# Performance work log

Hardware: AMD Instinct MI355X
Metric: run time of the kernel (lower is better)

The kernel has to match this reference:

```python
import jax, jax.numpy as jnp
import numpy as np

NUM_HEADS = 12
HEAD_DIM = 64


def setup_inputs() -> dict:
    key = jax.random.key(0)
    ks = jax.random.split(key, 8)
    B, S, D, M = 8, 1024, 768, 8
    scale = 0.02
    return {
        "hidden_states": jax.random.normal(ks[0], (B, S, D), jnp.float32),
        "memory": jax.random.normal(ks[1], (1, M, D), jnp.float32) * scale,
        "Wq": jax.random.normal(ks[2], (D, D), jnp.float32) * scale,
        "bq": jnp.zeros((D,), jnp.float32),
        "Wk": jax.random.normal(ks[3], (D, D), jnp.float32) * scale,
        "bk": jnp.zeros((D,), jnp.float32),
        "Wv": jax.random.normal(ks[4], (D, D), jnp.float32) * scale,
        "bv": jnp.zeros((D,), jnp.float32),
    }


def _split_heads(x):
    # (B, S, D) -> (B, H, S, Dh)
    B, S, _ = x.shape
    return x.reshape(B, S, NUM_HEADS, HEAD_DIM).transpose(0, 2, 1, 3)


def reference(hidden_states, memory, Wq, bq, Wk, bk, Wv, bv):
    B, S, D = hidden_states.shape
    # prepend? no: memory tokens are concatenated AFTER hidden_states on token dim
    mem = jnp.broadcast_to(memory, (B,) + memory.shape[1:])
    with_memory = jnp.concatenate([hidden_states, mem], axis=1)  # (B, S+M, D)

    # torch nn.Linear: x @ W.T + b
    q = _split_heads(hidden_states @ Wq.T + bq)   # (B, H, S,   Dh)
    k = _split_heads(with_memory @ Wk.T + bk)     # (B, H, S+M, Dh)
    v = _split_heads(with_memory @ Wv.T + bv)     # (B, H, S+M, Dh)

    scaling = 1.0 / np.sqrt(HEAD_DIM).astype(np.float32)
    scores = jnp.einsum("bhqd,bhkd->bhqk", q, k) * scaling
    probs = jax.nn.softmax(scores, axis=-1)  # dropout is identity in eval
    ctx = jnp.einsum("bhqk,bhkd->bhqd", probs, v)  # (B, H, S, Dh)
    ctx = ctx.transpose(0, 2, 1, 3).reshape(B, S, D)
    return ctx
```

## Files before the change

kernel.cpp:

```cpp
#include <hip/hip_runtime.h>

typedef unsigned short ushort_t;
typedef __attribute__((ext_vector_type(8))) short bf16x8;
typedef __attribute__((ext_vector_type(4))) short s16x4;
typedef __attribute__((ext_vector_type(4))) float f32x4;

#define BATCH 8
#define SEQ   1024
#define MEMT  8
#define LREAL 1032
#define LPAD  1152
#define DMODEL 768
#define NH    12
#define DH    64

#define CEXP 0.18033688011112042f

__device__ __forceinline__ ushort_t f2b(float x) {
  union { float f; unsigned u; } c; c.f = x;
  unsigned u = c.u;
  unsigned r = (u + 0x7fffu + ((u >> 16) & 1u)) >> 16;
  return (ushort_t)r;
}

#if defined(__has_builtin)
#if __has_builtin(__builtin_amdgcn_global_load_lds)
#define HAVE_GLL 1
#endif
#if __has_builtin(__builtin_amdgcn_exp2f)
#define EXP2F(x) __builtin_amdgcn_exp2f(x)
#endif
#endif
#ifndef EXP2F
#define EXP2F(x) __expf((x) * 0.6931471805599453f)
#endif

__device__ __forceinline__ void stage16(const ushort_t* g, ushort_t* lds_wave_base) {
#ifdef HAVE_GLL
  __builtin_amdgcn_global_load_lds(
      (const __attribute__((address_space(1))) unsigned int*)g,
      (__attribute__((address_space(3))) unsigned int*)lds_wave_base,
      16, 0, 0);
#else
  int lane = threadIdx.x & 63;
  *(bf16x8*)(lds_wave_base + lane * 8) = *(const bf16x8*)g;
#endif
}

__global__ __launch_bounds__(256) void prep(const float* __restrict__ hidden,
                                            const float* __restrict__ memv,
                                            const float* __restrict__ Wq,
                                            const float* __restrict__ Wk,
                                            const float* __restrict__ Wv,
                                            ushort_t* __restrict__ Xm,
                                            ushort_t* __restrict__ Wqb,
                                            ushort_t* __restrict__ Wkb,
                                            ushort_t* __restrict__ Wvb) {
  int bx = blockIdx.x;
  if (bx < 6912) {
    unsigned idx = ((unsigned)bx * 256u + threadIdx.x) * 4u;
    const unsigned perB = (unsigned)LPAD * DMODEL;
    unsigned b = idx / perB;
    unsigned rem = idx - b * perB;
    unsigned row = rem / DMODEL;
    unsigned col = rem - row * DMODEL;
    f32x4 v;
    if (row < SEQ) {
      v = *(const f32x4*)(hidden + ((size_t)b * SEQ + row) * DMODEL + col);
    } else if (row < LREAL) {
      v = *(const f32x4*)(memv + (size_t)(row - SEQ) * DMODEL + col);
    } else {
      v = (f32x4){0.f, 0.f, 0.f, 0.f};
    }
    s16x4 p;
    p[0] = (short)f2b(v[0]); p[1] = (short)f2b(v[1]);
    p[2] = (short)f2b(v[2]); p[3] = (short)f2b(v[3]);
    *(s16x4*)(Xm + idx) = p;
  } else {
    int t = bx - 6912;
    int m = t / 576;
    int i = (t - m * 576) * 256 + threadIdx.x;
    const float* src = m == 0 ? Wq : (m == 1 ? Wk : Wv);
    ushort_t* dst = m == 0 ? Wqb : (m == 1 ? Wkb : Wvb);
    f32x4 v = *(const f32x4*)(src + (size_t)i * 4);
    s16x4 p;
    p[0] = (short)f2b(v[0]); p[1] = (short)f2b(v[1]);
    p[2] = (short)f2b(v[2]); p[3] = (short)f2b(v[3]);
    *(s16x4*)(dst + (size_t)i * 4) = p;
  }
}

__global__ __launch_bounds__(512, 4) void gemm_fused(
    const ushort_t* __restrict__ Xm,
    const ushort_t* __restrict__ Wqb, const ushort_t* __restrict__ Wkb,
    const ushort_t* __restrict__ Wvb,
    const float* __restrict__ bq, const float* __restrict__ bk,
    const float* __restrict__ bv,
    ushort_t* __restrict__ Qb, ushort_t* __restrict__ Kb,
    ushort_t* __restrict__ Vtb) {
  __shared__ __align__(16) ushort_t S[17408];

  const int tid = threadIdx.x;
  const int wave = tid >> 6, lane = tid & 63;
  const int quad = lane >> 4, l15 = lane & 15;
  const int wm = wave >> 2, wn = wave & 3;
  const int lrow4 = lane >> 2, lcol8 = (lane & 3) << 3;

  int bx = blockIdx.x;
  int task, xt, yt, b;
  if (bx < 432) {
    int slot = bx & 7, rest = bx >> 3;
    int y = rest % 6, vhi = rest / 6;
    int v = slot + 8 * vhi;
    task = 2; xt = v % 9; b = v / 9; yt = y;
  } else if (bx < 816) {
    int t = bx - 432;
    int slot = t & 7, rest = t >> 3;
    int x = rest % 6, qhi = rest / 6;
    int q = slot + 8 * qhi;
    task = 0; xt = x; yt = q & 7; b = q >> 3;
  } else {
    int t = bx - 816;
    int slot = t & 7, rest = t >> 3;
    int x = rest % 6, khi = rest / 6;
    int k = slot + 8 * khi;
    task = 1; xt = x; yt = k % 9; b = k / 9;
  }
  const int rowTile = yt * 128, colTile = xt * 128;
  const ushort_t* Xb = Xm + (size_t)b * LPAD * DMODEL;
  const ushort_t* A = task == 2 ? Wvb : Xb;
  const ushort_t* W = task == 2 ? Xb : (task == 0 ? Wqb : Wkb);
  const float* bias = task == 2 ? bv : (task == 0 ? bq : bk);

  const ushort_t* Arow = A + (size_t)(rowTile + wave * 16 + lrow4) * DMODEL + lcol8;
  const ushort_t* Wrow = W + (size_t)(colTile + wave * 16 + lrow4) * DMODEL + lcol8;

  f32x4 acc[4][2] = {};

  stage16(Arow, S + wave * 512);
  stage16(Wrow, S + 4096 + wave * 512);
  __syncthreads();

  for (int i = 0; i < 24; ++i) {
    ushort_t* cur = S + ((i & 1) << 13);
    if (i < 23) {
      ushort_t* nxt = S + (((i + 1) & 1) << 13);
      int k0n = (i + 1) * 32;
      stage16(Arow + k0n, nxt + wave * 512);
      stage16(Wrow + k0n, nxt + 4096 + wave * 512);
    }
    bf16x8 af[4], bfr[2];
#pragma unroll
    for (int mt = 0; mt < 4; ++mt)
      af[mt] = *(const bf16x8*)&cur[(wm * 64 + mt * 16 + l15) * 32 + quad * 8];
#pragma unroll
    for (int nt = 0; nt < 2; ++nt)
      bfr[nt] = *(const bf16x8*)&cur[4096 + (wn * 32 + nt * 16 + l15) * 32 + quad * 8];
#pragma unroll
    for (int mt = 0; mt < 4; ++mt)
#pragma unroll
      for (int nt = 0; nt < 2; ++nt)
        acc[mt][nt] = __builtin_amdgcn_mfma_f32_16x16x32_bf16(af[mt], bfr[nt], acc[mt][nt], 0, 0, 0);
    __syncthreads();
  }

  const float scale = task == 0 ? CEXP : 1.0f;
#pragma unroll
  for (int mt = 0; mt < 4; ++mt)
#pragma unroll
    for (int nt = 0; nt < 2; ++nt) {
      int lr0 = wm * 64 + mt * 16 + quad * 4;
      int lc = wn * 32 + nt * 16 + l15;
#pragma unroll
      for (int r = 0; r < 4; ++r) {
        float bsv = (task == 2) ? bias[rowTile + lr0 + r] : bias[colTile + lc];
        S[(lr0 + r) * 136 + lc] = f2b((acc[mt][nt][r] + bsv) * scale);
      }
    }
  __syncthreads();

  {
    int row = tid >> 2;
    int segu = (tid & 3) * 32;
    bf16x8 v0 = *(const bf16x8*)&S[row * 136 + segu + 0];
    bf16x8 v1 = *(const bf16x8*)&S[row * 136 + segu + 8];
    bf16x8 v2 = *(const bf16x8*)&S[row * 136 + segu + 16];
    bf16x8 v3 = *(const bf16x8*)&S[row * 136 + segu + 24];
    if (task == 2) {
      int d = rowTile + row;
      ushort_t* gp = Vtb + (((size_t)b * NH + (d >> 6)) * DH + (d & 63)) * LPAD + colTile + segu;
      *(bf16x8*)(gp + 0) = v0;  *(bf16x8*)(gp + 8) = v1;
      *(bf16x8*)(gp + 16) = v2; *(bf16x8*)(gp + 24) = v3;
    } else {
      ushort_t* out = task == 0 ? Qb : Kb;
      const int Rows = task == 0 ? SEQ : LPAD;
      int colbase = colTile + segu;
      int h = colbase >> 6, dd = colbase & 63;
      ushort_t* gp = out + (((size_t)b * NH + h) * Rows + rowTile + row) * DH + dd;
      *(bf16x8*)(gp + 0) = v0;  *(bf16x8*)(gp + 8) = v1;
      *(bf16x8*)(gp + 16) = v2; *(bf16x8*)(gp + 24) = v3;
    }
  }
}

__global__ __launch_bounds__(256, 3) void attn(const ushort_t* __restrict__ Q,
                                               const ushort_t* __restrict__ K,
                                               const ushort_t* __restrict__ Vt,
                                               float* __restrict__ Out) {
  __shared__ __align__(16) ushort_t KV[16384];
  __shared__ __align__(16) ushort_t Ps[4 * 2304];

  const int tid = threadIdx.x, wave = tid >> 6, lane = tid & 63;
  const int quad = lane >> 4, l15 = lane & 15;
  const int lrow4 = lane >> 2, lcol8 = (lane & 3) << 3;
  const int bh = blockIdx.x, qt = blockIdx.y;
  const int h = bh % NH, b = bh / NH;

  const ushort_t* Qp = Q + (((size_t)b * NH + h) * SEQ + qt * 128) * DH;
  const ushort_t* Kp = K + ((size_t)b * NH + h) * LPAD * DH;
  const ushort_t* Vp = Vt + ((size_t)b * NH + h) * DH * LPAD;
  ushort_t* Pw = Ps + wave * 2304;

  bf16x8 qf[2][2];
#pragma unroll
  for (int mt = 0; mt < 2; ++mt)
#pragma unroll
    for (int kk = 0; kk < 2; ++kk)
      qf[mt][kk] = *(const bf16x8*)&Qp[(wave * 32 + mt * 16 + l15) * DH + kk * 32 + quad * 8];

  bf16x8 ones8;
#pragma unroll
  for (int j = 0; j < 8; ++j) ones8[j] = (short)0x3f80;

  f32x4 ob[2][4] = {};
  f32x4 obl[2] = {};

#define STAGE_KV(key0_, buf_)                                                        \
  {                                                                                  \
    _Pragma("unroll")                                                                \
    for (int s = 0; s < 2; ++s) {                                                    \
      int c = wave + s * 4;                                                          \
      int hi = c >> 2, lo = c & 3;                                                   \
      stage16(Kp + (size_t)((key0_) + lo * 16 + lrow4) * DH + hi * 32 + lcol8,       \
              (buf_) + c * 512);                                                     \
      stage16(Vp + (size_t)(lo * 16 + lrow4) * LPAD + (key0_) + hi * 32 + lcol8,     \
              (buf_) + 4096 + c * 512);                                              \
    }                                                                                \
  }

  STAGE_KV(0, KV)
  __syncthreads();

  for (int kt = 0; kt < 17; ++kt) {
    ushort_t* cur = KV + ((kt & 1) << 13);
    if (kt < 16) {
      ushort_t* nxt = KV + (((kt + 1) & 1) << 13);
      STAGE_KV((kt + 1) * 64, nxt)
    }

    f32x4 sc[2][4] = {};
#pragma unroll
    for (int kk = 0; kk < 2; ++kk)
#pragma unroll
      for (int nt = 0; nt < 4; ++nt) {
        bf16x8 kf = *(const bf16x8*)&cur[kk * 2048 + (nt * 16 + l15) * 32 + quad * 8];
#pragma unroll
        for (int mt = 0; mt < 2; ++mt)
          sc[mt][nt] = __builtin_amdgcn_mfma_f32_16x16x32_bf16(qf[mt][kk], kf, sc[mt][nt], 0, 0, 0);
      }

    if (kt < 16) {
#pragma unroll
      for (int mt = 0; mt < 2; ++mt)
#pragma unroll
        for (int nt = 0; nt < 4; ++nt)
#pragma unroll
          for (int r = 0; r < 4; ++r) {
            union { float f; unsigned u; } cu;
            cu.f = EXP2F(sc[mt][nt][r]);
            Pw[(mt * 16 + quad * 4 + r) * 72 + nt * 16 + l15] = (ushort_t)(cu.u >> 16);
          }
    } else {
      bool valid0 = (l15 < 8);
#pragma unroll
      for (int mt = 0; mt < 2; ++mt)
#pragma unroll
        for (int nt = 0; nt < 4; ++nt) {
          bool valid = (nt == 0) && valid0;
#pragma unroll
          for (int r = 0; r < 4; ++r) {
            union { float f; unsigned u; } cu;
            cu.f = valid ? EXP2F(sc[mt][nt][r]) : 0.f;
            Pw[(mt * 16 + quad * 4 + r) * 72 + nt * 16 + l15] = (ushort_t)(cu.u >> 16);
          }
        }
    }

#pragma unroll
    for (int kc = 0; kc < 2; ++kc) {
      bf16x8 pf[2];
#pragma unroll
      for (int mt = 0; mt < 2; ++mt)
        pf[mt] = *(const bf16x8*)&Pw[(mt * 16 + l15) * 72 + kc * 32 + quad * 8];
#pragma unroll
      for (int dt = 0; dt < 4; ++dt) {
        bf16x8 vf = *(const bf16x8*)&cur[4096 + kc * 2048 + (dt * 16 + l15) * 32 + quad * 8];
#pragma unroll
        for (int mt = 0; mt < 2; ++mt)
          ob[mt][dt] = __builtin_amdgcn_mfma_f32_16x16x32_bf16(pf[mt], vf, ob[mt][dt], 0, 0, 0);
      }
#pragma unroll
      for (int mt = 0; mt < 2; ++mt)
        obl[mt] = __builtin_amdgcn_mfma_f32_16x16x32_bf16(pf[mt], ones8, obl[mt], 0, 0, 0);
    }
    __syncthreads();
  }

#pragma unroll
  for (int mt = 0; mt < 2; ++mt) {
    int row0 = qt * 128 + wave * 32 + mt * 16 + quad * 4;
    f32x4 linv;
#pragma unroll
    for (int r = 0; r < 4; ++r) linv[r] = 1.0f / obl[mt][r];
#pragma unroll
    for (int dt = 0; dt < 4; ++dt) {
      int col = h * DH + dt * 16 + l15;
#pragma unroll
      for (int r = 0; r < 4; ++r)
        Out[((size_t)b * SEQ + row0 + r) * DMODEL + col] = ob[mt][dt][r] * linv[r];
    }
  }
}

extern "C" void kernel_launch(void* const* d_in, const int* in_sizes, int n_in,
                              void* d_out, int out_size, void* d_ws, size_t ws_size,
                              hipStream_t stream) {
  const float* hidden = (const float*)d_in[0];
  const float* memv   = (const float*)d_in[1];
  const float* Wq = (const float*)d_in[2];
  const float* bq = (const float*)d_in[3];
  const float* Wk = (const float*)d_in[4];
  const float* bk = (const float*)d_in[5];
  const float* Wv = (const float*)d_in[6];
  const float* bv = (const float*)d_in[7];
  float* out = (float*)d_out;

  char* ws = (char*)d_ws;
  size_t off = 0;
  ushort_t* Xm  = (ushort_t*)(ws + off); off += (size_t)BATCH * LPAD * DMODEL * 2;
  ushort_t* Wqb = (ushort_t*)(ws + off); off += (size_t)DMODEL * DMODEL * 2;
  ushort_t* Wkb = (ushort_t*)(ws + off); off += (size_t)DMODEL * DMODEL * 2;
  ushort_t* Wvb = (ushort_t*)(ws + off); off += (size_t)DMODEL * DMODEL * 2;
  ushort_t* Qb  = (ushort_t*)(ws + off); off += (size_t)BATCH * NH * SEQ * DH * 2;
  ushort_t* Kb  = (ushort_t*)(ws + off); off += (size_t)BATCH * NH * LPAD * DH * 2;
  ushort_t* Vtb = (ushort_t*)(ws + off);

  prep<<<dim3(8640), 256, 0, stream>>>(hidden, memv, Wq, Wk, Wv, Xm, Wqb, Wkb, Wvb);
  gemm_fused<<<dim3(1248), 512, 0, stream>>>(Xm, Wqb, Wkb, Wvb, bq, bk, bv, Qb, Kb, Vtb);
  attn<<<dim3(96, 8), 256, 0, stream>>>(Qb, Kb, Vtb, out);
}
```

Before: 180.5 us.

## Deepen projection GEMM pipeline to four LDS stages with swizzled layout

```diff
diff --git a/kernel.cpp b/kernel.cpp
--- a/kernel.cpp
+++ b/kernel.cpp
@@ -98,13 +98,13 @@
     const float* __restrict__ bv,
     ushort_t* __restrict__ Qb, ushort_t* __restrict__ Kb,
     ushort_t* __restrict__ Vtb) {
-  __shared__ __align__(16) ushort_t S[17408];
+  __shared__ __align__(16) ushort_t S[32768];
 
   const int tid = threadIdx.x;
   const int wave = tid >> 6, lane = tid & 63;
   const int quad = lane >> 4, l15 = lane & 15;
   const int wm = wave >> 2, wn = wave & 3;
-  const int lrow4 = lane >> 2, lcol8 = (lane & 3) << 3;
+  const int lrow4 = lane >> 2;
 
   int bx = blockIdx.x;
   int task, xt, yt, b;
@@ -132,37 +132,53 @@
   const ushort_t* W = task == 2 ? Xb : (task == 0 ? Wqb : Wkb);
   const float* bias = task == 2 ? bv : (task == 0 ? bq : bk);
 
-  const ushort_t* Arow = A + (size_t)(rowTile + wave * 16 + lrow4) * DMODEL + lcol8;
-  const ushort_t* Wrow = W + (size_t)(colTile + wave * 16 + lrow4) * DMODEL + lcol8;
+  const int swzcol = (((lane & 3) ^ ((lane >> 2) & 3)) << 3);
+  const ushort_t* Arow = A + (size_t)(rowTile + wave * 16 + lrow4) * DMODEL + swzcol;
+  const ushort_t* Wrow = W + (size_t)(colTile + wave * 16 + lrow4) * DMODEL + swzcol;
+
+  const int rds = (quad ^ (l15 & 3)) << 3;
+  const int rdA = (wm * 64 + l15) * 32 + rds;
+  const int rdB = 4096 + (wn * 32 + l15) * 32 + rds;
 
   f32x4 acc[4][2] = {};
 
-  stage16(Arow, S + wave * 512);
-  stage16(Wrow, S + 4096 + wave * 512);
-  __syncthreads();
-
-  for (int i = 0; i < 24; ++i) {
-    ushort_t* cur = S + ((i & 1) << 13);
-    if (i < 23) {
-      ushort_t* nxt = S + (((i + 1) & 1) << 13);
-      int k0n = (i + 1) * 32;
-      stage16(Arow + k0n, nxt + wave * 512);
-      stage16(Wrow + k0n, nxt + 4096 + wave * 512);
-    }
+#pragma unroll
+  for (int p = 0; p < 3; ++p) {
+    stage16(Arow + p * 32, S + p * 8192 + wave * 512);
+    stage16(Wrow + p * 32, S + p * 8192 + 4096 + wave * 512);
+  }
+  asm volatile("s_waitcnt vmcnt(4)" ::: "memory");
+  __builtin_amdgcn_s_barrier();
+  __builtin_amdgcn_sched_barrier(0);
+
+#pragma unroll 4
+  for (int kt = 0; kt < 24; ++kt) {
+    ushort_t* cur = S + (kt & 3) * 8192;
+    ushort_t* nxt = S + ((kt + 3) & 3) * 8192;
+    int kp = (kt + 3) * 32; if (kp > 736) kp = 736;
+    stage16(Arow + kp, nxt + wave * 512);
+    stage16(Wrow + kp, nxt + 4096 + wave * 512);
+
     bf16x8 af[4], bfr[2];
 #pragma unroll
     for (int mt = 0; mt < 4; ++mt)
-      af[mt] = *(const bf16x8*)&cur[(wm * 64 + mt * 16 + l15) * 32 + quad * 8];
+      af[mt] = *(const bf16x8*)&cur[rdA + mt * 512];
 #pragma unroll
     for (int nt = 0; nt < 2; ++nt)
-      bfr[nt] = *(const bf16x8*)&cur[4096 + (wn * 32 + nt * 16 + l15) * 32 + quad * 8];
+      bfr[nt] = *(const bf16x8*)&cur[rdB + nt * 512];
 #pragma unroll
     for (int mt = 0; mt < 4; ++mt)
 #pragma unroll
       for (int nt = 0; nt < 2; ++nt)
         acc[mt][nt] = __builtin_amdgcn_mfma_f32_16x16x32_bf16(af[mt], bfr[nt], acc[mt][nt], 0, 0, 0);
-    __syncthreads();
-  }
+
+    asm volatile("s_waitcnt vmcnt(4)" ::: "memory");
+    __builtin_amdgcn_s_barrier();
+    __builtin_amdgcn_sched_barrier(0);
+  }
+
+  asm volatile("s_waitcnt vmcnt(0)" ::: "memory");
+  __builtin_amdgcn_s_barrier();
 
   const float scale = task == 0 ? CEXP : 1.0f;
 #pragma unroll
```

Result: no change. 181.1 us (+0.3%).

## Enlarge QKV GEMM tiles to 128x256 and remap blocks per XCD

Applied to the files above, without the earlier changes.

```diff
diff --git a/kernel.cpp b/kernel.cpp
--- a/kernel.cpp
+++ b/kernel.cpp
@@ -90,7 +90,7 @@
   }
 }
 
-__global__ __launch_bounds__(512, 4) void gemm_fused(
+__global__ __launch_bounds__(512, 6) void gemm_fused(
     const ushort_t* __restrict__ Xm,
     const ushort_t* __restrict__ Wqb, const ushort_t* __restrict__ Wkb,
     const ushort_t* __restrict__ Wvb,
@@ -98,108 +98,140 @@
     const float* __restrict__ bv,
     ushort_t* __restrict__ Qb, ushort_t* __restrict__ Kb,
     ushort_t* __restrict__ Vtb) {
-  __shared__ __align__(16) ushort_t S[17408];
+  __shared__ __align__(16) ushort_t S[24576];
 
   const int tid = threadIdx.x;
   const int wave = tid >> 6, lane = tid & 63;
   const int quad = lane >> 4, l15 = lane & 15;
-  const int wm = wave >> 2, wn = wave & 3;
   const int lrow4 = lane >> 2, lcol8 = (lane & 3) << 3;
 
   int bx = blockIdx.x;
+  int g = (bx & 7) * 78 + (bx >> 3);
   int task, xt, yt, b;
-  if (bx < 432) {
-    int slot = bx & 7, rest = bx >> 3;
-    int y = rest % 6, vhi = rest / 6;
-    int v = slot + 8 * vhi;
-    task = 2; xt = v % 9; b = v / 9; yt = y;
-  } else if (bx < 816) {
-    int t = bx - 432;
-    int slot = t & 7, rest = t >> 3;
-    int x = rest % 6, qhi = rest / 6;
-    int q = slot + 8 * qhi;
-    task = 0; xt = x; yt = q & 7; b = q >> 3;
+  if (g < 192) {
+    task = 0; xt = g % 3; int r = g / 3; yt = r & 7; b = r >> 3;
+  } else if (g < 408) {
+    task = 1; int t = g - 192; xt = t % 3; int r = t / 3; yt = r % 9; b = r / 9;
   } else {
-    int t = bx - 816;
-    int slot = t & 7, rest = t >> 3;
-    int x = rest % 6, khi = rest / 6;
-    int k = slot + 8 * khi;
-    task = 1; xt = x; yt = k % 9; b = k / 9;
-  }
-  const int rowTile = yt * 128, colTile = xt * 128;
+    task = 2; int t = g - 408; xt = t % 9; int r = t / 9; yt = r % 3; b = r / 3;
+  }
+
+  const int BM = (task < 2) ? 128 : 256;
+  const int nA = BM >> 4;
+  const int bmEl = BM * 32;
+  const int rowTile = (task < 2) ? yt * 128 : yt * 256;
+  const int colTile = (task < 2) ? xt * 256 : xt * 128;
+
   const ushort_t* Xb = Xm + (size_t)b * LPAD * DMODEL;
   const ushort_t* A = task == 2 ? Wvb : Xb;
-  const ushort_t* W = task == 2 ? Xb : (task == 0 ? Wqb : Wkb);
+  const ushort_t* Bsrc = task == 2 ? Xb : (task == 0 ? Wqb : Wkb);
   const float* bias = task == 2 ? bv : (task == 0 ? bq : bk);
 
-  const ushort_t* Arow = A + (size_t)(rowTile + wave * 16 + lrow4) * DMODEL + lcol8;
-  const ushort_t* Wrow = W + (size_t)(colTile + wave * 16 + lrow4) * DMODEL + lcol8;
-
-  f32x4 acc[4][2] = {};
-
-  stage16(Arow, S + wave * 512);
-  stage16(Wrow, S + 4096 + wave * 512);
+  const ushort_t* Abase = A + (size_t)rowTile * DMODEL;
+  const ushort_t* Bbase = Bsrc + (size_t)colTile * DMODEL;
+
+  int wm, wn, wnCnt;
+  if (task < 2) { wm = wave >> 2; wn = wave & 3; wnCnt = 4; }
+  else          { wm = wave >> 1; wn = wave & 1; wnCnt = 2; }
+  (void)wnCnt;
+
+  const ushort_t* sp[3]; int lo[3];
+#pragma unroll
+  for (int s = 0; s < 3; ++s) {
+    int c = wave + s * 8;
+    bool isA = c < nA;
+    int cb = isA ? c : c - nA;
+    sp[s] = (isA ? Abase : Bbase) + (size_t)(cb * 16 + lrow4) * DMODEL + lcol8;
+    lo[s] = (isA ? 0 : bmEl) + cb * 512;
+  }
+
+  const int rdA = (wm * 64 + l15) * 32 + quad * 8;
+  const int rdB = bmEl + (wn * 64 + l15) * 32 + quad * 8;
+
+  f32x4 acc[4][4] = {};
+
+#pragma unroll
+  for (int s = 0; s < 3; ++s) stage16(sp[s], S + lo[s]);
   __syncthreads();
 
   for (int i = 0; i < 24; ++i) {
-    ushort_t* cur = S + ((i & 1) << 13);
+    ushort_t* cur = S + (i & 1) * 12288;
     if (i < 23) {
-      ushort_t* nxt = S + (((i + 1) & 1) << 13);
-      int k0n = (i + 1) * 32;
-      stage16(Arow + k0n, nxt + wave * 512);
-      stage16(Wrow + k0n, nxt + 4096 + wave * 512);
-    }
-    bf16x8 af[4], bfr[2];
+      ushort_t* nb = S + ((i + 1) & 1) * 12288;
+      int k0 = (i + 1) * 32;
+#pragma unroll
+      for (int s = 0; s < 3; ++s) stage16(sp[s] + k0, nb + lo[s]);
+    }
+    bf16x8 af[4], bf[4];
 #pragma unroll
     for (int mt = 0; mt < 4; ++mt)
-      af[mt] = *(const bf16x8*)&cur[(wm * 64 + mt * 16 + l15) * 32 + quad * 8];
-#pragma unroll
-    for (int nt = 0; nt < 2; ++nt)
-      bfr[nt] = *(const bf16x8*)&cur[4096 + (wn * 32 + nt * 16 + l15) * 32 + quad * 8];
+      af[mt] = *(const bf16x8*)&cur[rdA + mt * 512];
+#pragma unroll
+    for (int nt = 0; nt < 4; ++nt)
+      bf[nt] = *(const bf16x8*)&cur[rdB + nt * 512];
 #pragma unroll
     for (int mt = 0; mt < 4; ++mt)
 #pragma unroll
-      for (int nt = 0; nt < 2; ++nt)
-        acc[mt][nt] = __builtin_amdgcn_mfma_f32_16x16x32_bf16(af[mt], bfr[nt], acc[mt][nt], 0, 0, 0);
+      for (int nt = 0; nt < 4; ++nt)
+        acc[mt][nt] = __builtin_amdgcn_mfma_f32_16x16x32_bf16(af[mt], bf[nt], acc[mt][nt], 0, 0, 0);
     __syncthreads();
   }
 
   const float scale = task == 0 ? CEXP : 1.0f;
 #pragma unroll
-  for (int mt = 0; mt < 4; ++mt)
-#pragma unroll
-    for (int nt = 0; nt < 2; ++nt) {
-      int lr0 = wm * 64 + mt * 16 + quad * 4;
-      int lc = wn * 32 + nt * 16 + l15;
-#pragma unroll
-      for (int r = 0; r < 4; ++r) {
-        float bsv = (task == 2) ? bias[rowTile + lr0 + r] : bias[colTile + lc];
-        S[(lr0 + r) * 136 + lc] = f2b((acc[mt][nt][r] + bsv) * scale);
+  for (int h = 0; h < 2; ++h) {
+    bool part = (task < 2) ? ((wn >> 1) == h) : ((wm >> 1) == h);
+    if (part) {
+#pragma unroll
+      for (int mt = 0; mt < 4; ++mt)
+#pragma unroll
+        for (int nt = 0; nt < 4; ++nt) {
+          int ir0, ic;
+          float bsv;
+          if (task < 2) {
+            ir0 = wm * 64 + mt * 16 + quad * 4;
+            ic = (wn & 1) * 64 + nt * 16 + l15;
+            bsv = bias[colTile + h * 128 + ic];
+#pragma unroll
+            for (int r = 0; r < 4; ++r)
+              S[(ir0 + r) * 136 + ic] = f2b((acc[mt][nt][r] + bsv) * scale);
+          } else {
+            ir0 = (wm & 1) * 64 + mt * 16 + quad * 4;
+            ic = wn * 64 + nt * 16 + l15;
+#pragma unroll
+            for (int r = 0; r < 4; ++r) {
+              bsv = bias[rowTile + h * 128 + ir0 + r];
+              S[(ir0 + r) * 136 + ic] = f2b(acc[mt][nt][r] + bsv);
+            }
+          }
+        }
+    }
+    __syncthreads();
+
+    {
+      int row = tid >> 2;
+      int segu = (tid & 3) * 32;
+      bf16x8 v0 = *(const bf16x8*)&S[row * 136 + segu + 0];
+      bf16x8 v1 = *(const bf16x8*)&S[row * 136 + segu + 8];
+      bf16x8 v2 = *(const bf16x8*)&S[row * 136 + segu + 16];
+      bf16x8 v3 = *(const bf16x8*)&S[row * 136 + segu + 24];
+      if (task == 2) {
+        int d = rowTile + h * 128 + row;
+        int tok = colTile + segu;
+        ushort_t* gp = Vtb + (((size_t)b * NH + (d >> 6)) * DH + (d & 63)) * LPAD + tok;
+        *(bf16x8*)(gp + 0) = v0;  *(bf16x8*)(gp + 8) = v1;
+        *(bf16x8*)(gp + 16) = v2; *(bf16x8*)(gp + 24) = v3;
+      } else {
+        ushort_t* out = task == 0 ? Qb : Kb;
+        const int Rows = task == 0 ? SEQ : LPAD;
+        int colbase = colTile + h * 128 + segu;
+        int hd = colbase >> 6, dd = colbase & 63;
+        ushort_t* gp = out + (((size_t)b * NH + hd) * Rows + rowTile + row) * DH + dd;
+        *(bf16x8*)(gp + 0) = v0;  *(bf16x8*)(gp + 8) = v1;
+        *(bf16x8*)(gp + 16) = v2; *(bf16x8*)(gp + 24) = v3;
       }
     }
-  __syncthreads();
-
-  {
-    int row = tid >> 2;
-    int segu = (tid & 3) * 32;
-    bf16x8 v0 = *(const bf16x8*)&S[row * 136 + segu + 0];
-    bf16x8 v1 = *(const bf16x8*)&S[row * 136 + segu + 8];
-    bf16x8 v2 = *(const bf16x8*)&S[row * 136 + segu + 16];
-    bf16x8 v3 = *(const bf16x8*)&S[row * 136 + segu + 24];
-    if (task == 2) {
-      int d = rowTile + row;
-      ushort_t* gp = Vtb + (((size_t)b * NH + (d >> 6)) * DH + (d & 63)) * LPAD + colTile + segu;
-      *(bf16x8*)(gp + 0) = v0;  *(bf16x8*)(gp + 8) = v1;
-      *(bf16x8*)(gp + 16) = v2; *(bf16x8*)(gp + 24) = v3;
-    } else {
-      ushort_t* out = task == 0 ? Qb : Kb;
-      const int Rows = task == 0 ? SEQ : LPAD;
-      int colbase = colTile + segu;
-      int h = colbase >> 6, dd = colbase & 63;
-      ushort_t* gp = out + (((size_t)b * NH + h) * Rows + rowTile + row) * DH + dd;
-      *(bf16x8*)(gp + 0) = v0;  *(bf16x8*)(gp + 8) = v1;
-      *(bf16x8*)(gp + 16) = v2; *(bf16x8*)(gp + 24) = v3;
-    }
+    if (h == 0) __syncthreads();
   }
 }
 
@@ -356,6 +388,6 @@
   ushort_t* Vtb = (ushort_t*)(ws + off);
 
   prep<<<dim3(8640), 256, 0, stream>>>(hidden, memv, Wq, Wk, Wv, Xm, Wqb, Wkb, Wvb);
-  gemm_fused<<<dim3(1248), 512, 0, stream>>>(Xm, Wqb, Wkb, Wvb, bq, bk, bv, Qb, Kb, Vtb);
+  gemm_fused<<<dim3(624), 512, 0, stream>>>(Xm, Wqb, Wkb, Wvb, bq, bk, bv, Qb, Kb, Vtb);
   attn<<<dim3(96, 8), 256, 0, stream>>>(Qb, Kb, Vtb, out);
 }
```

New measurement: 321.8 us. 1.78x slower.
